# Performance work log

Hardware: AMD Instinct MI355X
Metric: run time of the kernel (lower is better)

## Reference

```python
import jax, jax.numpy as jnp
import numpy as np

B, L = 2, 1024
D_MODEL, N_LAYER, VOCAB = 768, 4, 32000
D_INNER, D_STATE, D_CONV = 2 * D_MODEL, 16, 4
DT_RANK = (D_MODEL + 15) // 16  # 48


def setup_inputs() -> dict:
    key = jax.random.key(0)
    ks = jax.random.split(key, 8)
    s = 0.02
    nl = N_LAYER
    A_init = jnp.tile(jnp.log(jnp.arange(1.0, D_STATE + 1.0, dtype=jnp.float32))[None, None, :], (nl, D_INNER, 1))
    return {
        "sequence": jax.random.randint(ks[0], (B, L), 0, VOCAB),
        "sequence_mask": jnp.ones((B, L), dtype=jnp.int32),
        "emb": jax.random.normal(ks[1], (VOCAB, D_MODEL)) * s,
        "norm_w": jnp.ones((nl, D_MODEL)),
        "in_proj_w": jax.random.normal(ks[2], (nl, 2 * D_INNER, D_MODEL)) * s,
        "conv_w": jax.random.normal(ks[3], (nl, D_INNER, D_CONV)) * s,
        "conv_b": jnp.zeros((nl, D_INNER)),
        "x_proj_w": jax.random.normal(ks[4], (nl, DT_RANK + 2 * D_STATE, D_INNER)) * s,
        "dt_w": jax.random.normal(ks[5], (nl, D_INNER, DT_RANK)) * s,
        "dt_b": jnp.log(jnp.expm1(jnp.full((nl, D_INNER), 1e-2))),  # inv-softplus(dt_init)
        "A_log": A_init,
        "D_skip": jnp.ones((nl, D_INNER)),
        "out_w": jax.random.normal(ks[6], (nl, D_MODEL, D_INNER)) * s,
        "normf_w": jnp.ones((D_MODEL,)),
    }


def _rmsnorm(x, w, eps=1e-5):
    x = x.astype(jnp.float32)
    return x * jax.lax.rsqrt(jnp.mean(x * x, axis=-1, keepdims=True) + eps) * w


def _mamba_block(h, in_w, cw, cb, xpw, dtw, dtb, a_log, d_skip, ow):
    # h: [B, L, D_MODEL]
    Bsz, Lsz, _ = h.shape
    xz = jnp.einsum('bld,ed->ble', h, in_w)  # [B, L, 2*d_inner]
    x, z = jnp.split(xz, 2, axis=-1)
    # causal depthwise conv1d, kernel D_CONV
    xp = jnp.pad(x, ((0, 0), (D_CONV - 1, 0), (0, 0)))
    x = sum(xp[:, k:k + Lsz, :] * cw[:, k] for k in range(D_CONV)) + cb
    x = jax.nn.silu(x)
    xdbl = jnp.einsum('bld,ed->ble', x, xpw)  # [B, L, dt_rank + 2*d_state]
    dt = xdbl[..., :DT_RANK]
    Bm = xdbl[..., DT_RANK:DT_RANK + D_STATE]
    Cm = xdbl[..., DT_RANK + D_STATE:]
    delta = jax.nn.softplus(jnp.einsum('blr,dr->bld', dt, dtw) + dtb)  # [B, L, d_inner]
    A = -jnp.exp(a_log)  # [d_inner, d_state]

    def step(hstate, inp):
        d_t, b_t, c_t, u_t = inp  # [B,di],[B,ds],[B,ds],[B,di]
        dA = jnp.exp(d_t[..., None] * A)  # [B, di, ds]
        hstate = dA * hstate + (d_t * u_t)[..., None] * b_t[:, None, :]
        y = jnp.einsum('bds,bs->bd', hstate, c_t)
        return hstate, y

    h0 = jnp.zeros((Bsz, D_INNER, D_STATE), dtype=x.dtype)
    _, ys = jax.lax.scan(
        step, h0,
        (delta.transpose(1, 0, 2), Bm.transpose(1, 0, 2), Cm.transpose(1, 0, 2), x.transpose(1, 0, 2)))
    y = ys.transpose(1, 0, 2) + x * d_skip
    y = y * jax.nn.silu(z)
    return jnp.einsum('bld,ed->ble', y, ow)


def _forward(sequence, sequence_mask, emb, norm_w, in_proj_w, conv_w, conv_b,
             x_proj_w, dt_w, dt_b, A_log, D_skip, out_w, normf_w):
    residual = emb[sequence]  # [B, L, D]
    for i in range(norm_w.shape[0]):
        hn = _rmsnorm(residual, norm_w[i])
        residual = residual + _mamba_block(hn, in_proj_w[i], conv_w[i], conv_b[i],
                                           x_proj_w[i], dt_w[i], dt_b[i],
                                           A_log[i], D_skip[i], out_w[i])
    out = _rmsnorm(residual, normf_w)  # [B, L, D]
    last = sequence_mask.sum(-1).astype(jnp.int32) - 1
    return out[jnp.arange(out.shape[0]), last]  # [B, D] last valid hidden state


def reference(sequence, sequence_mask, emb, norm_w, in_proj_w, conv_w, conv_b,
              x_proj_w, dt_w, dt_b, A_log, D_skip, out_w, normf_w):
    return _forward(sequence, sequence_mask, emb, norm_w, in_proj_w, conv_w, conv_b,
                    x_proj_w, dt_w, dt_b, A_log, D_skip, out_w, normf_w)
```

## Files before the change

kernel.cpp:

```cpp
#include <hip/hip_runtime.h>
#include <hip/hip_bf16.h>

#define BSZ 2
#define LSEQ 1024
#define DMODEL 768
#define NLAYER 4
#define DINNER 1536
#define DSTATE 16
#define DCONV 4
#define DTRANK 48
#define NCHUNK 64
#define CLEN 16
#define XDSTR 128
#define XZLD (2 * DINNER)

typedef __bf16 bf16x8_t __attribute__((ext_vector_type(8)));
typedef float f32x4_t __attribute__((ext_vector_type(4)));
typedef unsigned short u16x8_t __attribute__((ext_vector_type(8)));
typedef __hip_bfloat16 bf16;

__device__ inline float bfbits2f(unsigned short u) {
    unsigned int x = ((unsigned int)u) << 16;
    return __builtin_bit_cast(float, x);
}
__device__ inline unsigned short f2bfbits(float f) {
    return __builtin_bit_cast(unsigned short, (__bf16)f);
}

__device__ __forceinline__ void gload16(const bf16* g, bf16* l) {
    __builtin_amdgcn_global_load_lds(
        (const __attribute__((address_space(1))) unsigned int*)g,
        (__attribute__((address_space(3))) unsigned int*)l,
        16, 0, 0);
}

__device__ inline float block_reduce_sum(float v, float* sbuf) {
    __syncthreads();
    #pragma unroll
    for (int o = 32; o > 0; o >>= 1) v += __shfl_down(v, o, 64);
    int wid = threadIdx.x >> 6;
    int lane = threadIdx.x & 63;
    if (lane == 0) sbuf[wid] = v;
    __syncthreads();
    if (threadIdx.x == 0) sbuf[0] = (sbuf[0] + sbuf[1]) + (sbuf[2] + sbuf[3]);
    __syncthreads();
    return sbuf[0];
}

#define PN1 (NLAYER * 3072 * 768)
#define PN2 (NLAYER * 768 * 1536)
#define PN3 (NLAYER * 128 * 1536)
#define PN4 (BSZ * LSEQ * DMODEL)
#define PN5 (2 * BSZ * LSEQ * XDSTR)
__global__ __launch_bounds__(256) void init_kernel(
    const int* __restrict__ seq, const float* __restrict__ emb,
    const float* __restrict__ in_w, const float* __restrict__ out_w,
    const float* __restrict__ xp_w,
    float* __restrict__ residual, bf16* __restrict__ in16,
    bf16* __restrict__ out16, bf16* __restrict__ xp16, float* __restrict__ xdbl2) {
    int idx = blockIdx.x * 256 + threadIdx.x;
    if (idx < PN1) { in16[idx] = __float2bfloat16(in_w[idx]); return; }
    idx -= PN1;
    if (idx < PN2) { out16[idx] = __float2bfloat16(out_w[idx]); return; }
    idx -= PN2;
    if (idx < PN3) {
        int l = idx / (128 * DINNER);
        int r = idx - l * (128 * DINNER);
        int e = r / DINNER;
        int k = r - e * DINNER;
        xp16[idx] = (e < 80) ? __float2bfloat16(xp_w[((size_t)l * 80 + e) * DINNER + k])
                             : __float2bfloat16(0.f);
        return;
    }
    idx -= PN3;
    if (idx < PN4) {
        int bl = idx / DMODEL;
        int dd = idx - bl * DMODEL;
        residual[idx] = emb[(size_t)seq[bl] * DMODEL + dd];
        return;
    }
    idx -= PN4;
    xdbl2[idx] = 0.f;
}

__global__ __launch_bounds__(256) void rmsnorm_kernel(
    const float* __restrict__ res, const float* __restrict__ w, bf16* __restrict__ out) {
    __shared__ float sbuf[8];
    int row = blockIdx.x;
    const float* x = res + (size_t)row * DMODEL;
    float ss = 0.f;
    for (int i = threadIdx.x; i < DMODEL; i += 256) { float v = x[i]; ss += v * v; }
    ss = block_reduce_sum(ss, sbuf);
    float scale = rsqrtf(ss / (float)DMODEL + 1e-5f);
    for (int i = threadIdx.x; i < DMODEL; i += 256)
        out[(size_t)row * DMODEL + i] = __float2bfloat16(x[i] * scale * w[i]);
}

__global__ __launch_bounds__(256) void rmsnorm_acc_kernel(
    float* __restrict__ res, const float* __restrict__ p0, const float* __restrict__ p1,
    const float* __restrict__ p2, const float* __restrict__ p3,
    const float* __restrict__ w, bf16* __restrict__ out) {
    __shared__ float sbuf[8];
    int row = blockIdx.x;
    size_t base = (size_t)row * DMODEL;
    float ss = 0.f;
    for (int i = threadIdx.x; i < DMODEL; i += 256) {
        float v = res[base + i] + ((p0[base + i] + p1[base + i]) + (p2[base + i] + p3[base + i]));
        res[base + i] = v;
        ss += v * v;
    }
    ss = block_reduce_sum(ss, sbuf);
    float scale = rsqrtf(ss / (float)DMODEL + 1e-5f);
    for (int i = threadIdx.x; i < DMODEL; i += 256)
        out[base + i] = __float2bfloat16(res[base + i] * scale * w[i]);
}

__global__ __launch_bounds__(256) void gemm_128x64_g(
    const bf16* __restrict__ A, int lda, const bf16* __restrict__ Bw, int ldb,
    bf16* __restrict__ C16, int ldc, int K) {
    __shared__ bf16 As[128][64];
    __shared__ bf16 Bs[64][64];
    int tid = threadIdx.x;
    int wave = tid >> 6;
    int lane = tid & 63;
    int quad = lane >> 4;
    int l16 = lane & 15;
    int bm = blockIdx.x * 128;
    int bn = blockIdx.y * 64;
    int wm = wave * 32;
    int lr = lane >> 3;
    int lc = (lane & 7) ^ lr;
    int sx = (l16 & 7) << 3;

    f32x4_t acc[2][4];
    #pragma unroll
    for (int i = 0; i < 2; ++i)
        #pragma unroll
        for (int j = 0; j < 4; ++j) acc[i][j] = (f32x4_t){0.f, 0.f, 0.f, 0.f};

    for (int k0 = 0; k0 < K; k0 += 64) {
        #pragma unroll
        for (int i = 0; i < 6; ++i) {
            int ch = wave * 6 + i;
            if (ch < 16) {
                int r = ch * 8 + lr;
                gload16(A + (size_t)(bm + r) * lda + k0 + lc * 8, &As[ch * 8][0]);
            } else {
                int c2 = ch - 16;
                int r = c2 * 8 + lr;
                gload16(Bw + (size_t)(bn + r) * ldb + k0 + lc * 8, &Bs[c2 * 8][0]);
            }
        }
        __syncthreads();
        #pragma unroll
        for (int kk = 0; kk < 64; kk += 32) {
            bf16x8_t af[2], bf[4];
            #pragma unroll
            for (int i = 0; i < 2; ++i)
                af[i] = *(const bf16x8_t*)(&As[wm + i * 16 + l16][(kk + quad * 8) ^ sx]);
            #pragma unroll
            for (int j = 0; j < 4; ++j)
                bf[j] = *(const bf16x8_t*)(&Bs[j * 16 + l16][(kk + quad * 8) ^ sx]);
            #pragma unroll
            for (int i = 0; i < 2; ++i)
                #pragma unroll
                for (int j = 0; j < 4; ++j)
                    acc[i][j] = __builtin_amdgcn_mfma_f32_16x16x32_bf16(af[i], bf[j], acc[i][j], 0, 0, 0);
        }
        __syncthreads();
    }

    int mbase = bm + wm + quad * 4;
    #pragma unroll
    for (int i = 0; i < 2; ++i)
        #pragma unroll
        for (int j = 0; j < 4; ++j) {
            int n = bn + j * 16 + l16;
            #pragma unroll
            for (int r = 0; r < 4; ++r)
                C16[(size_t)(mbase + i * 16 + r) * ldc + n] = __float2bfloat16(acc[i][j][r]);
        }
}

__global__ __launch_bounds__(256) void gemm_64_atomic_g(
    const bf16* __restrict__ A, int lda, const bf16* __restrict__ Bw, int ldb,
    float* __restrict__ Cf, int ldc, int K) {
    __shared__ bf16 As[64][64];
    __shared__ bf16 Bs[64][64];
    int tid = threadIdx.x;
    int wave = tid >> 6;
    int lane = tid & 63;
    int quad = lane >> 4;
    int l16 = lane & 15;
    int bm = blockIdx.x * 64;
    int bn = blockIdx.y * 64;
    int lr = lane >> 3;
    int lc = (lane & 7) ^ lr;
    int sx = (l16 & 7) << 3;
    int kpb = K / gridDim.z;
    int kbeg = blockIdx.z * kpb;
    int kend = kbeg + kpb;

    f32x4_t acc[4];
    #pragma unroll
    for (int i = 0; i < 4; ++i) acc[i] = (f32x4_t){0.f, 0.f, 0.f, 0.f};

    for (int k0 = kbeg; k0 < kend; k0 += 64) {
        #pragma unroll
        for (int i = 0; i < 4; ++i) {
            int ch = wave * 4 + i;
            if (ch < 8) {
                int r = ch * 8 + lr;
                gload16(A + (size_t)(bm + r) * lda + k0 + lc * 8, &As[ch * 8][0]);
            } else {
                int c2 = ch - 8;
                int r = c2 * 8 + lr;
                gload16(Bw + (size_t)(bn + r) * ldb + k0 + lc * 8, &Bs[c2 * 8][0]);
            }
        }
        __syncthreads();
        #pragma unroll
        for (int kk = 0; kk < 64; kk += 32) {
            bf16x8_t af = *(const bf16x8_t*)(&As[wave * 16 + l16][(kk + quad * 8) ^ sx]);
            #pragma unroll
            for (int i = 0; i < 4; ++i) {
                bf16x8_t bv = *(const bf16x8_t*)(&Bs[i * 16 + l16][(kk + quad * 8) ^ sx]);
                acc[i] = __builtin_amdgcn_mfma_f32_16x16x32_bf16(af, bv, acc[i], 0, 0, 0);
            }
        }
        __syncthreads();
    }

    int m0 = bm + wave * 16 + quad * 4;
    #pragma unroll
    for (int i = 0; i < 4; ++i) {
        int n = bn + i * 16 + l16;
        #pragma unroll
        for (int r = 0; r < 4; ++r)
            atomicAdd(&Cf[(size_t)(m0 + r) * ldc + n], acc[i][r]);
    }
}

__global__ __launch_bounds__(256) void gemm_128x64_part_g(
    const bf16* __restrict__ A, int lda, const bf16* __restrict__ Bw, int ldb,
    float* __restrict__ P0, float* __restrict__ P1,
    float* __restrict__ P2, float* __restrict__ P3, int ldc, int K) {
    __shared__ bf16 As[128][64];
    __shared__ bf16 Bs[64][64];
    int tid = threadIdx.x;
    int wave = tid >> 6;
    int lane = tid & 63;
    int quad = lane >> 4;
    int l16 = lane & 15;
    int bm = blockIdx.x * 128;
    int bn = blockIdx.y * 64;
    int wm = wave * 32;
    int lr = lane >> 3;
    int lc = (lane & 7) ^ lr;
    int sx = (l16 & 7) << 3;
    int kpb = K / 4;
    int kbeg = blockIdx.z * kpb;
    int kend = kbeg + kpb;
    float* Cf = (blockIdx.z == 0) ? P0 : (blockIdx.z == 1) ? P1 : (blockIdx.z == 2) ? P2 : P3;

    f32x4_t acc[2][4];
    #pragma unroll
    for (int i = 0; i < 2; ++i)
        #pragma unroll
        for (int j = 0; j < 4; ++j) acc[i][j] = (f32x4_t){0.f, 0.f, 0.f, 0.f};

    for (int k0 = kbeg; k0 < kend; k0 += 64) {
        #pragma unroll
        for (int i = 0; i < 6; ++i) {
            int ch = wave * 6 + i;
            if (ch < 16) {
                int r = ch * 8 + lr;
                gload16(A + (size_t)(bm + r) * lda + k0 + lc * 8, &As[ch * 8][0]);
            } else {
                int c2 = ch - 16;
                int r = c2 * 8 + lr;
                gload16(Bw + (size_t)(bn + r) * ldb + k0 + lc * 8, &Bs[c2 * 8][0]);
            }
        }
        __syncthreads();
        #pragma unroll
        for (int kk = 0; kk < 64; kk += 32) {
            bf16x8_t af[2], bf[4];
            #pragma unroll
            for (int i = 0; i < 2; ++i)
                af[i] = *(const bf16x8_t*)(&As[wm + i * 16 + l16][(kk + quad * 8) ^ sx]);
            #pragma unroll
            for (int j = 0; j < 4; ++j)
                bf[j] = *(const bf16x8_t*)(&Bs[j * 16 + l16][(kk + quad * 8) ^ sx]);
            #pragma unroll
            for (int i = 0; i < 2; ++i)
                #pragma unroll
                for (int j = 0; j < 4; ++j)
                    acc[i][j] = __builtin_amdgcn_mfma_f32_16x16x32_bf16(af[i], bf[j], acc[i][j], 0, 0, 0);
        }
        __syncthreads();
    }

    int mbase = bm + wm + quad * 4;
    #pragma unroll
    for (int i = 0; i < 2; ++i)
        #pragma unroll
        for (int j = 0; j < 4; ++j) {
            int n = bn + j * 16 + l16;
            #pragma unroll
            for (int r = 0; r < 4; ++r)
                Cf[(size_t)(mbase + i * 16 + r) * ldc + n] = acc[i][j][r];
        }
}

#define UCHUNKS (DINNER / 8)
__global__ __launch_bounds__(256) void usilu_kernel(
    const bf16* __restrict__ xz16, const float* __restrict__ cw, const float* __restrict__ cb,
    bf16* __restrict__ u16) {
    int idx = blockIdx.x * 256 + threadIdx.x;
    int row = idx / UCHUNKS;
    int d0 = (idx - row * UCHUNKS) * 8;
    int l = row & (LSEQ - 1);
    const u16x8_t Z8 = (u16x8_t){0, 0, 0, 0, 0, 0, 0, 0};
    u16x8_t xa[4];
    #pragma unroll
    for (int t = 0; t < 4; ++t)
        xa[t] = (l >= 3 - t) ? *(const u16x8_t*)(xz16 + (size_t)(row - 3 + t) * XZLD + d0) : Z8;
    u16x8_t r;
    #pragma unroll
    for (int j = 0; j < 8; ++j) {
        float4 cwv = *(const float4*)(cw + (size_t)(d0 + j) * 4);
        float a = cb[d0 + j]
            + bfbits2f(xa[0][j]) * cwv.x + bfbits2f(xa[1][j]) * cwv.y
            + bfbits2f(xa[2][j]) * cwv.z + bfbits2f(xa[3][j]) * cwv.w;
        a = a / (1.f + __expf(-a));
        r[j] = f2bfbits(a);
    }
    *(u16x8_t*)(u16 + (size_t)row * DINNER + d0) = r;
}

__device__ inline float compute_delta(const float* __restrict__ xrow,
                                      const float* __restrict__ dtw, float dtbd) {
    float acc = dtbd;
    #pragma unroll
    for (int j = 0; j < DTRANK; j += 4) {
        float4 xv = *(const float4*)(xrow + j);
        acc += xv.x * dtw[j] + xv.y * dtw[j + 1] + xv.z * dtw[j + 2] + xv.w * dtw[j + 3];
    }
    return (acc > 20.f) ? acc : log1pf(__expf(acc));
}

__global__ __launch_bounds__(256) void scan_phaseA(
    const bf16* __restrict__ u16, const float* __restrict__ xdbl,
    const float* __restrict__ dt_w, const float* __restrict__ dt_b,
    const float* __restrict__ A_log,
    float* __restrict__ Psum, float* __restrict__ Ssum,
    float* __restrict__ Dbuf,
    float* __restrict__ xd_next) {
    int gtid = blockIdx.x * 256 + threadIdx.x;
    int d = gtid % DINNER;
    int c = (gtid / DINNER) % NCHUNK;
    int b = gtid / (DINNER * NCHUNK);
    float dtw[DTRANK];
    #pragma unroll
    for (int j = 0; j < DTRANK; j += 4)
        *(float4*)(dtw + j) = *(const float4*)(dt_w + (size_t)d * DTRANK + j);
    float dtbd = dt_b[d];
    float Av[DSTATE], P[DSTATE], S[DSTATE];
    #pragma unroll
    for (int s = 0; s < DSTATE; ++s) {
        Av[s] = -__expf(A_log[d * DSTATE + s]);
        P[s] = 1.f; S[s] = 0.f;
    }
    int t0 = c * CLEN;
    int rowb = b * LSEQ;
    for (int i = 0; i < CLEN; ++i) {
        int row = rowb + t0 + i;
        const float* xrow = xdbl + (size_t)row * XDSTR;
        float dl = compute_delta(xrow, dtw, dtbd);
        Dbuf[(size_t)row * DINNER + d] = dl;
        float u = __bfloat162float(u16[(size_t)row * DINNER + d]);
        float bt = dl * u;
        const float4* Bp = (const float4*)(xrow + DTRANK);
        float4 B0 = Bp[0], B1 = Bp[1], B2 = Bp[2], B3 = Bp[3];
        float Bv[DSTATE] = {B0.x,B0.y,B0.z,B0.w, B1.x,B1.y,B1.z,B1.w,
                            B2.x,B2.y,B2.z,B2.w, B3.x,B3.y,B3.z,B3.w};
        #pragma unroll
        for (int s = 0; s < DSTATE; ++s) {
            float a = __expf(dl * Av[s]);
            P[s] *= a;
            S[s] = a * S[s] + bt * Bv[s];
        }
    }
    size_t base = ((size_t)(b * NCHUNK + c) * DSTATE) * DINNER + d;
    #pragma unroll
    for (int s = 0; s < DSTATE; ++s) {
        Psum[base + (size_t)s * DINNER] = P[s];
        Ssum[base + (size_t)s * DINNER] = S[s];
    }
    for (int z = gtid; z < BSZ * LSEQ * XDSTR; z += BSZ * NCHUNK * DINNER)
        xd_next[z] = 0.f;
}

__global__ __launch_bounds__(256) void scan_phaseB(
    float* __restrict__ Psum, const float* __restrict__ Ssum) {
    int gtid = blockIdx.x * 256 + threadIdx.x;
    int d = gtid % DINNER;
    int s = (gtid / DINNER) % DSTATE;
    int b = gtid / (DINNER * DSTATE);
    float h = 0.f;
    for (int c = 0; c < NCHUNK; ++c) {
        size_t idx = ((size_t)(b * NCHUNK + c) * DSTATE + s) * DINNER + d;
        float p = Psum[idx];
        Psum[idx] = h;
        h = p * h + Ssum[idx];
    }
}

__global__ __launch_bounds__(256) void scan_phaseC(
    bf16* __restrict__ uy16, const bf16* __restrict__ xz16,
    const float* __restrict__ xdbl,
    const float* __restrict__ A_log, const float* __restrict__ D_skip,
    const float* __restrict__ H0, const float* __restrict__ Dbuf) {
    int gtid = blockIdx.x * 256 + threadIdx.x;
    int d = gtid % DINNER;
    int c = (gtid / DINNER) % NCHUNK;
    int b = gtid / (DINNER * NCHUNK);
    float Av[DSTATE], h[DSTATE];
    size_t base = ((size_t)(b * NCHUNK + c) * DSTATE) * DINNER + d;
    #pragma unroll
    for (int s = 0; s < DSTATE; ++s) {
        Av[s] = -__expf(A_log[d * DSTATE + s]);
        h[s] = H0[base + (size_t)s * DINNER];
    }
    float Dsk = D_skip[d];
    int t0 = c * CLEN;
    int rowb = b * LSEQ;
    for (int i = 0; i < CLEN; ++i) {
        int row = rowb + t0 + i;
        const float* xrow = xdbl + (size_t)row * XDSTR;
        float dl = Dbuf[(size_t)row * DINNER + d];
        float u = __bfloat162float(uy16[(size_t)row * DINNER + d]);
        float bt = dl * u;
        const float4* Bp = (const float4*)(xrow + DTRANK);
        float4 B0 = Bp[0], B1 = Bp[1], B2 = Bp[2], B3 = Bp[3];
        const float4* Cp = (const float4*)(xrow + DTRANK + DSTATE);
        float4 C0 = Cp[0], C1 = Cp[1], C2 = Cp[2], C3 = Cp[3];
        float Bv[DSTATE] = {B0.x,B0.y,B0.z,B0.w, B1.x,B1.y,B1.z,B1.w,
                            B2.x,B2.y,B2.z,B2.w, B3.x,B3.y,B3.z,B3.w};
        float Cv[DSTATE] = {C0.x,C0.y,C0.z,C0.w, C1.x,C1.y,C1.z,C1.w,
                            C2.x,C2.y,C2.z,C2.w, C3.x,C3.y,C3.z,C3.w};
        float acc = 0.f;
        #pragma unroll
        for (int s = 0; s < DSTATE; ++s) {
            float a = __expf(dl * Av[s]);
            h[s] = a * h[s] + bt * Bv[s];
            acc += h[s] * Cv[s];
        }
        float zv = __bfloat162float(xz16[(size_t)row * XZLD + DINNER + d]);
        float sz = zv / (1.f + __expf(-zv));
        uy16[(size_t)row * DINNER + d] = __float2bfloat16((acc + u * Dsk) * sz);
    }
}

__global__ __launch_bounds__(256) void final_acc_kernel(
    const float* __restrict__ res, const float* __restrict__ p0, const float* __restrict__ p1,
    const float* __restrict__ p2, const float* __restrict__ p3,
    const int* __restrict__ mask, const float* __restrict__ w, float* __restrict__ out) {
    __shared__ float sbuf[8];
    int b = blockIdx.x;
    float cnt = 0.f;
    for (int i = threadIdx.x; i < LSEQ; i += 256) cnt += (float)mask[b * LSEQ + i];
    cnt = block_reduce_sum(cnt, sbuf);
    int last = (int)cnt - 1;
    size_t base = ((size_t)b * LSEQ + last) * DMODEL;
    float ss = 0.f;
    for (int i = threadIdx.x; i < DMODEL; i += 256) {
        float v = res[base + i] + ((p0[base + i] + p1[base + i]) + (p2[base + i] + p3[base + i]));
        ss += v * v;
    }
    ss = block_reduce_sum(ss, sbuf);
    float scale = rsqrtf(ss / (float)DMODEL + 1e-5f);
    for (int i = threadIdx.x; i < DMODEL; i += 256) {
        float v = res[base + i] + ((p0[base + i] + p1[base + i]) + (p2[base + i] + p3[base + i]));
        out[b * DMODEL + i] = v * scale * w[i];
    }
}

extern "C" void kernel_launch(void* const* d_in, const int* in_sizes, int n_in,
                              void* d_out, int out_size, void* d_ws, size_t ws_size,
                              hipStream_t stream) {
    const int*   seq      = (const int*)d_in[0];
    const int*   mask     = (const int*)d_in[1];
    const float* emb      = (const float*)d_in[2];
    const float* norm_w   = (const float*)d_in[3];
    const float* in_w     = (const float*)d_in[4];
    const float* conv_w   = (const float*)d_in[5];
    const float* conv_b   = (const float*)d_in[6];
    const float* xp_w     = (const float*)d_in[7];
    const float* dt_w     = (const float*)d_in[8];
    const float* dt_b     = (const float*)d_in[9];
    const float* A_log    = (const float*)d_in[10];
    const float* D_skip   = (const float*)d_in[11];
    const float* out_w    = (const float*)d_in[12];
    const float* normf_w  = (const float*)d_in[13];
    float* out = (float*)d_out;

    char* ws = (char*)d_ws;
    float* residual = (float*)(ws);
    bf16*  hn16     = (bf16*)(ws + 6291456);
    bf16*  xz16     = (bf16*)(ws + 9437184);
    float* xdbl     = (float*)(ws + 22020096);
    bf16*  uy16     = (bf16*)(ws + 24117248);
    float* Psum     = (float*)(ws + 30408704);
    float* Ssum     = (float*)(ws + 42991616);
    float* Dbuf     = (float*)(ws + 55574528);
    bf16*  in16     = (bf16*)(ws + 68157440);
    bf16*  out16    = (bf16*)(ws + 87031808);
    bf16*  xp16     = (bf16*)(ws + 96468992);
    float* P0 = Psum;
    float* P1 = Psum + (size_t)BSZ * LSEQ * DMODEL;
    float* P2 = Ssum;
    float* P3 = Ssum + (size_t)BSZ * LSEQ * DMODEL;

    init_kernel<<<66560, 256, 0, stream>>>(seq, emb, in_w, out_w, xp_w,
                                           residual, in16, out16, xp16, xdbl);

    for (int i = 0; i < NLAYER; ++i) {
        float* xd_cur = xdbl + (size_t)(i & 1) * (BSZ * LSEQ * XDSTR);
        float* xd_nxt = xdbl + (size_t)((i + 1) & 1) * (BSZ * LSEQ * XDSTR);
        const float* cw = conv_w + (size_t)i * DINNER * DCONV;
        const float* cb = conv_b + (size_t)i * DINNER;
        const float* dw = dt_w + (size_t)i * DINNER * DTRANK;
        const float* db = dt_b + (size_t)i * DINNER;
        const float* al = A_log + (size_t)i * DINNER * DSTATE;

        if (i == 0)
            rmsnorm_kernel<<<BSZ * LSEQ, 256, 0, stream>>>(
                residual, norm_w, hn16);
        else
            rmsnorm_acc_kernel<<<BSZ * LSEQ, 256, 0, stream>>>(
                residual, P0, P1, P2, P3, norm_w + (size_t)i * DMODEL, hn16);
        gemm_128x64_g<<<dim3(16, 48), 256, 0, stream>>>(
            hn16, DMODEL, in16 + (size_t)i * 3072 * DMODEL, DMODEL, xz16, XZLD, DMODEL);
        usilu_kernel<<<(BSZ * LSEQ * UCHUNKS) / 256, 256, 0, stream>>>(xz16, cw, cb, uy16);
        gemm_64_atomic_g<<<dim3(32, 2, 8), 256, 0, stream>>>(
            uy16, DINNER, xp16 + (size_t)i * 128 * DINNER, DINNER, xd_cur, XDSTR, DINNER);
        scan_phaseA<<<768, 256, 0, stream>>>(
            uy16, xd_cur, dw, db, al, Psum, Ssum, Dbuf, xd_nxt);
        scan_phaseB<<<192, 256, 0, stream>>>(Psum, Ssum);
        scan_phaseC<<<768, 256, 0, stream>>>(
            uy16, xz16, xd_cur, al, D_skip + (size_t)i * DINNER, Psum, Dbuf);
        gemm_128x64_part_g<<<dim3(16, 12, 4), 256, 0, stream>>>(
            uy16, DINNER, out16 + (size_t)i * DMODEL * DINNER, DINNER,
            P0, P1, P2, P3, DMODEL, DINNER);
    }

    final_acc_kernel<<<BSZ, 256, 0, stream>>>(residual, P0, P1, P2, P3, mask, normf_w, out);
}
```

Before: 702.7 us.

## Double-buffer shared-memory tiles in GEMM kernels to overlap loads with MFMA

Converts the three GEMM kernels from single-buffered to double-buffered shared-memory tiles. The next K-tile is issued into the alternate buffer before computing on the current one, leaving one barrier per iteration instead of two. This aims to hide global-to-LDS load latency behind matrix-core work, at the cost of doubled LDS usage per block, which may reduce occupancy. Correctness depends on gload16 completing before the barrier, as before.

```diff
diff --git a/kernel.cpp b/kernel.cpp
--- a/kernel.cpp
+++ b/kernel.cpp
@@ -118,8 +118,8 @@
 __global__ __launch_bounds__(256) void gemm_128x64_g(
     const bf16* __restrict__ A, int lda, const bf16* __restrict__ Bw, int ldb,
     bf16* __restrict__ C16, int ldc, int K) {
-    __shared__ bf16 As[128][64];
-    __shared__ bf16 Bs[64][64];
+    __shared__ bf16 As[2][128][64];
+    __shared__ bf16 Bs[2][64][64];
     int tid = threadIdx.x;
     int wave = tid >> 6;
     int lane = tid & 63;
@@ -138,37 +138,48 @@
         #pragma unroll
         for (int j = 0; j < 4; ++j) acc[i][j] = (f32x4_t){0.f, 0.f, 0.f, 0.f};
 
-    for (int k0 = 0; k0 < K; k0 += 64) {
+    auto stage = [&](int k0, int pb) {
         #pragma unroll
         for (int i = 0; i < 6; ++i) {
             int ch = wave * 6 + i;
             if (ch < 16) {
                 int r = ch * 8 + lr;
-                gload16(A + (size_t)(bm + r) * lda + k0 + lc * 8, &As[ch * 8][0]);
+                gload16(A + (size_t)(bm + r) * lda + k0 + lc * 8, &As[pb][ch * 8][0]);
             } else {
                 int c2 = ch - 16;
                 int r = c2 * 8 + lr;
-                gload16(Bw + (size_t)(bn + r) * ldb + k0 + lc * 8, &Bs[c2 * 8][0]);
+                gload16(Bw + (size_t)(bn + r) * ldb + k0 + lc * 8, &Bs[pb][c2 * 8][0]);
             }
         }
-        __syncthreads();
+    };
+    auto compute = [&](int pb) {
         #pragma unroll
         for (int kk = 0; kk < 64; kk += 32) {
             bf16x8_t af[2], bf[4];
             #pragma unroll
             for (int i = 0; i < 2; ++i)
-                af[i] = *(const bf16x8_t*)(&As[wm + i * 16 + l16][(kk + quad * 8) ^ sx]);
+                af[i] = *(const bf16x8_t*)(&As[pb][wm + i * 16 + l16][(kk + quad * 8) ^ sx]);
             #pragma unroll
             for (int j = 0; j < 4; ++j)
-                bf[j] = *(const bf16x8_t*)(&Bs[j * 16 + l16][(kk + quad * 8) ^ sx]);
+                bf[j] = *(const bf16x8_t*)(&Bs[pb][j * 16 + l16][(kk + quad * 8) ^ sx]);
             #pragma unroll
             for (int i = 0; i < 2; ++i)
                 #pragma unroll
                 for (int j = 0; j < 4; ++j)
                     acc[i][j] = __builtin_amdgcn_mfma_f32_16x16x32_bf16(af[i], bf[j], acc[i][j], 0, 0, 0);
         }
+    };
+
+    stage(0, 0);
+    __syncthreads();
+    int cur = 0;
+    for (int k0 = 64; k0 < K; k0 += 64) {
+        stage(k0, cur ^ 1);
+        compute(cur);
         __syncthreads();
-    }
+        cur ^= 1;
+    }
+    compute(cur);
 
     int mbase = bm + wm + quad * 4;
     #pragma unroll
@@ -185,8 +196,8 @@
 __global__ __launch_bounds__(256) void gemm_64_atomic_g(
     const bf16* __restrict__ A, int lda, const bf16* __restrict__ Bw, int ldb,
     float* __restrict__ Cf, int ldc, int K) {
-    __shared__ bf16 As[64][64];
-    __shared__ bf16 Bs[64][64];
+    __shared__ bf16 As[2][64][64];
+    __shared__ bf16 Bs[2][64][64];
     int tid = threadIdx.x;
     int wave = tid >> 6;
     int lane = tid & 63;
@@ -205,31 +216,42 @@
     #pragma unroll
     for (int i = 0; i < 4; ++i) acc[i] = (f32x4_t){0.f, 0.f, 0.f, 0.f};
 
-    for (int k0 = kbeg; k0 < kend; k0 += 64) {
+    auto stage = [&](int k0, int pb) {
         #pragma unroll
         for (int i = 0; i < 4; ++i) {
             int ch = wave * 4 + i;
             if (ch < 8) {
                 int r = ch * 8 + lr;
-                gload16(A + (size_t)(bm + r) * lda + k0 + lc * 8, &As[ch * 8][0]);
+                gload16(A + (size_t)(bm + r) * lda + k0 + lc * 8, &As[pb][ch * 8][0]);
             } else {
                 int c2 = ch - 8;
                 int r = c2 * 8 + lr;
-                gload16(Bw + (size_t)(bn + r) * ldb + k0 + lc * 8, &Bs[c2 * 8][0]);
+                gload16(Bw + (size_t)(bn + r) * ldb + k0 + lc * 8, &Bs[pb][c2 * 8][0]);
             }
         }
-        __syncthreads();
+    };
+    auto compute = [&](int pb) {
         #pragma unroll
         for (int kk = 0; kk < 64; kk += 32) {
-            bf16x8_t af = *(const bf16x8_t*)(&As[wave * 16 + l16][(kk + quad * 8) ^ sx]);
+            bf16x8_t af = *(const bf16x8_t*)(&As[pb][wave * 16 + l16][(kk + quad * 8) ^ sx]);
             #pragma unroll
             for (int i = 0; i < 4; ++i) {
-                bf16x8_t bv = *(const bf16x8_t*)(&Bs[i * 16 + l16][(kk + quad * 8) ^ sx]);
+                bf16x8_t bv = *(const bf16x8_t*)(&Bs[pb][i * 16 + l16][(kk + quad * 8) ^ sx]);
                 acc[i] = __builtin_amdgcn_mfma_f32_16x16x32_bf16(af, bv, acc[i], 0, 0, 0);
             }
         }
+    };
+
+    stage(kbeg, 0);
+    __syncthreads();
+    int cur = 0;
+    for (int k0 = kbeg + 64; k0 < kend; k0 += 64) {
+        stage(k0, cur ^ 1);
+        compute(cur);
         __syncthreads();
-    }
+        cur ^= 1;
+    }
+    compute(cur);
 
     int m0 = bm + wave * 16 + quad * 4;
     #pragma unroll
@@ -245,8 +267,8 @@
     const bf16* __restrict__ A, int lda, const bf16* __restrict__ Bw, int ldb,
     float* __restrict__ P0, float* __restrict__ P1,
     float* __restrict__ P2, float* __restrict__ P3, int ldc, int K) {
-    __shared__ bf16 As[128][64];
-    __shared__ bf16 Bs[64][64];
+    __shared__ bf16 As[2][128][64];
+    __shared__ bf16 Bs[2][64][64];
     int tid = threadIdx.x;
     int wave = tid >> 6;
     int lane = tid & 63;
@@ -269,37 +291,48 @@
         #pragma unroll
         for (int j = 0; j < 4; ++j) acc[i][j] = (f32x4_t){0.f, 0.f, 0.f, 0.f};
 
-    for (int k0 = kbeg; k0 < kend; k0 += 64) {
+    auto stage = [&](int k0, int pb) {
         #pragma unroll
         for (int i = 0; i < 6; ++i) {
             int ch = wave * 6 + i;
             if (ch < 16) {
                 int r = ch * 8 + lr;
-                gload16(A + (size_t)(bm + r) * lda + k0 + lc * 8, &As[ch * 8][0]);
+                gload16(A + (size_t)(bm + r) * lda + k0 + lc * 8, &As[pb][ch * 8][0]);
             } else {
                 int c2 = ch - 16;
                 int r = c2 * 8 + lr;
-                gload16(Bw + (size_t)(bn + r) * ldb + k0 + lc * 8, &Bs[c2 * 8][0]);
+                gload16(Bw + (size_t)(bn + r) * ldb + k0 + lc * 8, &Bs[pb][c2 * 8][0]);
             }
         }
-        __syncthreads();
+    };
+    auto compute = [&](int pb) {
         #pragma unroll
         for (int kk = 0; kk < 64; kk += 32) {
             bf16x8_t af[2], bf[4];
             #pragma unroll
             for (int i = 0; i < 2; ++i)
-                af[i] = *(const bf16x8_t*)(&As[wm + i * 16 + l16][(kk + quad * 8) ^ sx]);
+                af[i] = *(const bf16x8_t*)(&As[pb][wm + i * 16 + l16][(kk + quad * 8) ^ sx]);
             #pragma unroll
             for (int j = 0; j < 4; ++j)
-                bf[j] = *(const bf16x8_t*)(&Bs[j * 16 + l16][(kk + quad * 8) ^ sx]);
+                bf[j] = *(const bf16x8_t*)(&Bs[pb][j * 16 + l16][(kk + quad * 8) ^ sx]);
             #pragma unroll
             for (int i = 0; i < 2; ++i)
                 #pragma unroll
                 for (int j = 0; j < 4; ++j)
                     acc[i][j] = __builtin_amdgcn_mfma_f32_16x16x32_bf16(af[i], bf[j], acc[i][j], 0, 0, 0);
         }
+    };
+
+    stage(kbeg, 0);
+    __syncthreads();
+    int cur = 0;
+    for (int k0 = kbeg + 64; k0 < kend; k0 += 64) {
+        stage(k0, cur ^ 1);
+        compute(cur);
         __syncthreads();
-    }
+        cur ^= 1;
+    }
+    compute(cur);
 
     int mbase = bm + wm + quad * 4;
     #pragma unroll
```

After: 687.0 us. 2.2% less time.
